# Kernel optimization log

Hardware: AMD Instinct MI355X
Metric: run time of the kernel (lower is better)

Reference implementation:

```python
import jax, jax.numpy as jnp
import numpy as np
import math

B, T, D, H = 4, 2048, 1024, 16
DH = D // H

def setup_inputs() -> dict:
    key = jax.random.key(0)
    ks = jax.random.split(key, 5)
    scale = 1.0 / math.sqrt(D)
    x = jax.random.normal(ks[0], (B, T, D), dtype=jnp.float32)
    Wq = jax.random.normal(ks[1], (D, D), dtype=jnp.float32) * scale
    Wk = jax.random.normal(ks[2], (D, D), dtype=jnp.float32) * scale
    Wv = jax.random.normal(ks[3], (D, D), dtype=jnp.float32) * scale
    Wo = jax.random.normal(ks[4], (D, D), dtype=jnp.float32) * scale
    mask = jnp.tril(jnp.ones((T, T), dtype=jnp.int32))  # causal, 1=keep
    return {"x": x, "mask": mask, "Wq": Wq, "Wk": Wk, "Wv": Wv, "Wo": Wo}

def reference(x, mask, Wq, Wk, Wv, Wo):
    Bx, Tx, Dx = x.shape
    # nn.Linear(bias=False): y = x @ W.T
    q = (x @ Wq.T).reshape(Bx, Tx, H, DH).transpose(0, 2, 1, 3)  # [B,H,T,dh]
    k = (x @ Wk.T).reshape(Bx, Tx, H, DH).transpose(0, 2, 1, 3)
    v = (x @ Wv.T).reshape(Bx, Tx, H, DH).transpose(0, 2, 1, 3)
    scores = jnp.einsum('bhqd,bhkd->bhqk', q, k) / math.sqrt(DH)
    m = mask[None, None, :, :]  # [1,1,T,T]
    scores = scores + (m == 0).astype(scores.dtype) * -1e9
    attn = jax.nn.softmax(scores, axis=-1)  # stable (max-subtract) like original
    out = jnp.einsum('bhqk,bhkd->bhqd', attn, v)
    out = out.transpose(0, 2, 1, 3).reshape(Bx, Tx, Dx)
    return out @ Wo.T
```

## Files before the change

### kernel.cpp

```cpp
#include <hip/hip_runtime.h>
#include <stdint.h>

#define B_  4
#define T_  2048
#define D_  1024
#define H_  16
#define DH_ 64

typedef unsigned short u16;
typedef __attribute__((ext_vector_type(8))) short bf16x8;
typedef __attribute__((ext_vector_type(8))) unsigned short u16x8;
typedef __attribute__((ext_vector_type(4))) unsigned short u16x4;
typedef __attribute__((ext_vector_type(4))) float f32x4;

#define NT_ ((size_t)B_ * T_ * D_)
#define QSCALE 0.18033688011112043f

__device__ __forceinline__ u16 f2bf(float f) {
    union { float f; uint32_t u; } v; v.f = f;
    uint32_t r = v.u + 0x7FFFu + ((v.u >> 16) & 1u);
    return (u16)(r >> 16);
}

__device__ __forceinline__ uint32_t pack2(float lo, float hi) {
    union { float f; uint32_t u; } a, b; a.f = lo; b.f = hi;
    return __builtin_amdgcn_perm(b.u, a.u, 0x07060302u);
}

__device__ __forceinline__ void gl2lds16(const u16* g, u16* l) {
    __builtin_amdgcn_global_load_lds(
        (const __attribute__((address_space(1))) unsigned int*)g,
        (__attribute__((address_space(3))) unsigned int*)l,
        16, 0, 0);
}

__global__ __launch_bounds__(256) void cvt_x_kernel(
    const float* __restrict__ src, u16* __restrict__ dst, int n8)
{
    int i = blockIdx.x * 256 + threadIdx.x;
    if (i >= n8) return;
    f32x4 a = ((const f32x4*)src)[2 * i];
    f32x4 b = ((const f32x4*)src)[2 * i + 1];
    u16x8 o;
    o[0]=f2bf(a[0]); o[1]=f2bf(a[1]); o[2]=f2bf(a[2]); o[3]=f2bf(a[3]);
    o[4]=f2bf(b[0]); o[5]=f2bf(b[1]); o[6]=f2bf(b[2]); o[7]=f2bf(b[3]);
    ((u16x8*)dst)[i] = o;
}

__global__ __launch_bounds__(256) void cvt_w_kernel(
    const float* __restrict__ w0, const float* __restrict__ w1,
    const float* __restrict__ w2, const float* __restrict__ w3,
    u16* __restrict__ dst)
{
    const float* src = (blockIdx.y == 0) ? w0 : (blockIdx.y == 1) ? w1
                     : (blockIdx.y == 2) ? w2 : w3;
    u16* d = dst + (size_t)blockIdx.y * (D_ * D_);
    int i = blockIdx.x * 256 + threadIdx.x;
    f32x4 a = ((const f32x4*)src)[2 * i];
    f32x4 b = ((const f32x4*)src)[2 * i + 1];
    u16x8 o;
    o[0]=f2bf(a[0]); o[1]=f2bf(a[1]); o[2]=f2bf(a[2]); o[3]=f2bf(a[3]);
    o[4]=f2bf(b[0]); o[5]=f2bf(b[1]); o[6]=f2bf(b[2]); o[7]=f2bf(b[3]);
    ((u16x8*)d)[i] = o;
}

template<int OUT_MODE>
__global__ __launch_bounds__(256) void gemm_bt_kernel(
    const u16* __restrict__ X, const u16* __restrict__ W,
    void* __restrict__ C, int M, int N, int K)
{
    __shared__ __align__(16) u16 As[128 * 64];
    __shared__ __align__(16) u16 Bs[128 * 64];

    const int tid  = threadIdx.x;
    const int wave = tid >> 6;
    const int lane = tid & 63;
    const int lq = lane >> 4;
    const int lm = lane & 15;
    const int m0 = blockIdx.x * 128;
    const int n0 = blockIdx.y * 128;
    const int wm = (wave & 1) * 64;
    const int wn = (wave >> 1) * 64;

    f32x4 acc[4][4] = {};

    const int r0 = wave * 32 + (lane >> 3);
    const int c0 = (lane & 7) * 8;
    const u16* gA = X + (size_t)(m0 + r0) * K + c0;
    const u16* gB = W + (size_t)(n0 + r0) * K + c0;
    u16* lA = As + wave * 32 * 64;
    u16* lB = Bs + wave * 32 * 64;

    for (int k0 = 0; k0 < K; k0 += 64) {
#pragma unroll
        for (int p = 0; p < 4; ++p) {
            gl2lds16(gA + (size_t)p * 8 * K + k0, lA + p * 8 * 64);
            gl2lds16(gB + (size_t)p * 8 * K + k0, lB + p * 8 * 64);
        }
        __syncthreads();
#pragma unroll
        for (int ks = 0; ks < 2; ++ks) {
            bf16x8 af[4], bfr[4];
#pragma unroll
            for (int t = 0; t < 4; ++t)
                af[t] = *(const bf16x8*)(As + (wm + t * 16 + lm) * 64 + ks * 32 + lq * 8);
#pragma unroll
            for (int t = 0; t < 4; ++t)
                bfr[t] = *(const bf16x8*)(Bs + (wn + t * 16 + lm) * 64 + ks * 32 + lq * 8);
#pragma unroll
            for (int i = 0; i < 4; ++i)
#pragma unroll
                for (int j = 0; j < 4; ++j)
                    acc[i][j] = __builtin_amdgcn_mfma_f32_16x16x32_bf16(
                        af[i], bfr[j], acc[i][j], 0, 0, 0);
        }
        __syncthreads();
    }

    const int region = n0 >> 10;
#pragma unroll
    for (int i = 0; i < 4; ++i)
#pragma unroll
        for (int j = 0; j < 4; ++j) {
            int rowb = m0 + wm + i * 16 + lq * 4;
            int col  = n0 + wn + j * 16 + lm;
            if (OUT_MODE == 2) {
#pragma unroll
                for (int r = 0; r < 4; ++r)
                    ((float*)C)[(size_t)(rowb + r) * N + col] = acc[i][j][r];
            } else {
                u16* Qp = (u16*)C;
                int colr = col & 1023;
                if (region == 0) {
#pragma unroll
                    for (int r = 0; r < 4; ++r)
                        Qp[(size_t)(rowb + r) * D_ + colr] = f2bf(acc[i][j][r] * QSCALE);
                } else if (region == 1) {
#pragma unroll
                    for (int r = 0; r < 4; ++r)
                        (Qp + NT_)[(size_t)(rowb + r) * D_ + colr] = f2bf(acc[i][j][r]);
                } else {
                    int b = rowb >> 11, t = rowb & (T_ - 1);
                    u16x4 pk;
#pragma unroll
                    for (int r = 0; r < 4; ++r) pk[r] = f2bf(acc[i][j][r]);
                    *(u16x4*)((Qp + 2 * NT_) + ((size_t)b * D_ + colr) * T_ + t) = pk;
                }
            }
        }
}

__global__ __launch_bounds__(128) void attn_kernel(
    const u16* __restrict__ Qg, const u16* __restrict__ Kg,
    const u16* __restrict__ Vtg, u16* __restrict__ Og)
{
    __shared__ __align__(16) u16 Pl[2 * 64 * 40];
    __shared__ __align__(16) float Oc[16 * 64 * 4];
    __shared__ __align__(16) float Lc[4 * 64];

    const int tid  = threadIdx.x;
    const int wave = tid >> 6;
    const int lane = tid & 63;
    const int lq = lane >> 4, lm = lane & 15;
    const int id = blockIdx.x;
    const int xs = id & 7;
    const int k8 = id >> 3;
    const int bh = xs + 8 * (k8 & 7);
    const int pi = k8 >> 3;
    const int b = bh >> 4, h = bh & 15;

    const size_t batchoff = (size_t)b * T_ * D_;
    const size_t headoff  = (size_t)h * DH_;
    const size_t vbase    = (size_t)bh * DH_ * T_;

    u16* pw = Pl + wave * 64 * 40;

#pragma unroll 1
    for (int ph = 0; ph < 2; ++ph) {
        const int qj  = ph ? (31 - pi) : pi;
        const int qw  = qj * 64;
        const int ktd = qj >> 1;
        const int odd = qj & 1;

        bf16x8 aq[4][2];
#pragma unroll
        for (int qf = 0; qf < 4; ++qf) {
            const u16* qrow = Qg + batchoff + (size_t)(qw + qf * 16 + lm) * D_ + headoff;
            aq[qf][0] = *(const bf16x8*)(qrow + lq * 8);
            aq[qf][1] = *(const bf16x8*)(qrow + 32 + lq * 8);
        }

        f32x4 oaccT[4][4] = {};
        float l_lane[4] = {0.f, 0.f, 0.f, 0.f};

#pragma unroll 1
        for (int kt = wave; kt <= ktd; kt += 2) {
            const bool diag = (kt == ktd);
            const int ksmax = diag ? (odd ? 3 : 1) : 3;

#pragma unroll
            for (int c = 0; c < 4; ++c) {
                if (c <= ksmax) {
#pragma unroll
                    for (int t = 0; t < 2; ++t) {
                        const int mt = 2 * c + t;
                        const u16* krow = Kg + batchoff
                            + (size_t)(kt * 128 + mt * 16 + lm) * D_ + headoff;
                        bf16x8 kf0 = *(const bf16x8*)(krow + lq * 8);
                        bf16x8 kf1 = *(const bf16x8*)(krow + 32 + lq * 8);
                        f32x4 s[4];
#pragma unroll
                        for (int qf = 0; qf < 4; ++qf) {
                            s[qf] = f32x4{0.f, 0.f, 0.f, 0.f};
                            s[qf] = __builtin_amdgcn_mfma_f32_16x16x32_bf16(
                                kf0, aq[qf][0], s[qf], 0, 0, 0);
                            s[qf] = __builtin_amdgcn_mfma_f32_16x16x32_bf16(
                                kf1, aq[qf][1], s[qf], 0, 0, 0);
                        }
                        if (diag) {
                            int keyb = kt * 128 + mt * 16 + lq * 4;
#pragma unroll
                            for (int qf = 0; qf < 4; ++qf) {
                                int query = qw + qf * 16 + lm;
#pragma unroll
                                for (int r = 0; r < 4; ++r)
                                    if (keyb + r > query) s[qf][r] = -1e9f;
                            }
                        }
#pragma unroll
                        for (int qf = 0; qf < 4; ++qf) {
                            float p0 = __builtin_amdgcn_exp2f(s[qf][0]);
                            float p1 = __builtin_amdgcn_exp2f(s[qf][1]);
                            float p2 = __builtin_amdgcn_exp2f(s[qf][2]);
                            float p3 = __builtin_amdgcn_exp2f(s[qf][3]);
                            l_lane[qf] += (p0 + p1) + (p2 + p3);
                            uint2 d; d.x = pack2(p0, p1); d.y = pack2(p2, p3);
                            *(uint2*)(pw + (qf * 16 + lm) * 40 + t * 16 + lq * 4) = d;
                        }
                    }

                    bf16x8 pf[4];
#pragma unroll
                    for (int qf = 0; qf < 4; ++qf)
                        pf[qf] = *(const bf16x8*)(pw + (qf * 16 + lm) * 40 + lq * 8);
#pragma unroll
                    for (int mo = 0; mo < 4; ++mo) {
                        const u16* vrow = Vtg + vbase
                            + (size_t)(mo * 16 + lm) * T_ + kt * 128 + c * 32;
                        bf16x8 vf = *(const bf16x8*)(vrow + lq * 8);
#pragma unroll
                        for (int qf = 0; qf < 4; ++qf)
                            oaccT[qf][mo] = __builtin_amdgcn_mfma_f32_16x16x32_bf16(
                                vf, pf[qf], oaccT[qf][mo], 0, 0, 0);
                    }
                }
            }
        }

        if (wave == 1) {
#pragma unroll
            for (int qf = 0; qf < 4; ++qf) {
#pragma unroll
                for (int mo = 0; mo < 4; ++mo)
                    *(f32x4*)&Oc[((qf * 4 + mo) * 64 + lane) * 4] = oaccT[qf][mo];
                Lc[qf * 64 + lane] = l_lane[qf];
            }
        }
        __syncthreads();
        if (wave == 0) {
#pragma unroll
            for (int qf = 0; qf < 4; ++qf) {
#pragma unroll
                for (int mo = 0; mo < 4; ++mo) {
                    f32x4 o = *(const f32x4*)&Oc[((qf * 4 + mo) * 64 + lane) * 4];
#pragma unroll
                    for (int r = 0; r < 4; ++r) oaccT[qf][mo][r] += o[r];
                }
                l_lane[qf] += Lc[qf * 64 + lane];
            }
#pragma unroll
            for (int qf = 0; qf < 4; ++qf) {
                float l = l_lane[qf];
                l += __shfl_xor(l, 16, 64);
                l += __shfl_xor(l, 32, 64);
                float inv = 1.0f / l;
                int row = qw + qf * 16 + lm;
                u16* obase = Og + batchoff + (size_t)row * D_ + headoff;
#pragma unroll
                for (int mo = 0; mo < 4; ++mo) {
                    uint2 d;
                    d.x = pack2(oaccT[qf][mo][0] * inv, oaccT[qf][mo][1] * inv);
                    d.y = pack2(oaccT[qf][mo][2] * inv, oaccT[qf][mo][3] * inv);
                    *(uint2*)(obase + mo * 16 + lq * 4) = d;
                }
            }
        }
        __syncthreads();
    }
}

extern "C" void kernel_launch(void* const* d_in, const int* in_sizes, int n_in,
                              void* d_out, int out_size, void* d_ws, size_t ws_size,
                              hipStream_t stream)
{
    const float* x  = (const float*)d_in[0];
    const float* Wq = (const float*)d_in[2];
    const float* Wk = (const float*)d_in[3];
    const float* Wv = (const float*)d_in[4];
    const float* Wo = (const float*)d_in[5];

    const size_t DD = (size_t)D_ * D_;
    u16* Qb  = (u16*)d_ws;
    u16* Kb  = Qb + NT_;
    u16* Vb  = Kb + NT_;
    u16* Ob  = Vb + NT_;
    u16* xb  = Ob + NT_;
    u16* wb  = xb + NT_;

    const int M = B_ * T_;

    cvt_x_kernel<<<dim3((int)(NT_ / 8 / 256)), 256, 0, stream>>>(x, xb, (int)(NT_ / 8));
    cvt_w_kernel<<<dim3((int)(DD / 8 / 256), 4), 256, 0, stream>>>(Wq, Wk, Wv, Wo, wb);

    gemm_bt_kernel<3><<<dim3(M / 128, 3 * D_ / 128), 256, 0, stream>>>(
        xb, wb, Qb, M, 3 * D_, D_);

    attn_kernel<<<dim3(1024), 128, 0, stream>>>(Qb, Kb, Vb, Ob);

    gemm_bt_kernel<2><<<dim3(M / 128, D_ / 128), 256, 0, stream>>>(
        Ob, wb + 3 * DD, d_out, M, D_, D_);
}
```

Measured before the change: 289.5 us.

## Rewrite projection GEMM as 256x256 8-wave double-buffered pipelined kernel

```diff
diff --git a/kernel.cpp b/kernel.cpp
--- a/kernel.cpp
+++ b/kernel.cpp
@@ -33,6 +33,8 @@
         (__attribute__((address_space(3))) unsigned int*)l,
         16, 0, 0);
 }
+
+#define VMCNT(n) asm volatile("s_waitcnt vmcnt(" #n ")" ::: "memory")
 
 __global__ __launch_bounds__(256) void cvt_x_kernel(
     const float* __restrict__ src, u16* __restrict__ dst, int n8)
@@ -65,65 +67,129 @@
 }
 
 template<int OUT_MODE>
-__global__ __launch_bounds__(256) void gemm_bt_kernel(
+__global__ __launch_bounds__(512) void gemm8_kernel(
     const u16* __restrict__ X, const u16* __restrict__ W,
     void* __restrict__ C, int M, int N, int K)
 {
-    __shared__ __align__(16) u16 As[128 * 64];
-    __shared__ __align__(16) u16 Bs[128 * 64];
+    __shared__ __align__(16) u16 Ab2[2][256 * 64];
+    __shared__ __align__(16) u16 Bb2[2][256 * 64];
 
     const int tid  = threadIdx.x;
     const int wave = tid >> 6;
     const int lane = tid & 63;
-    const int lq = lane >> 4;
-    const int lm = lane & 15;
-    const int m0 = blockIdx.x * 128;
-    const int n0 = blockIdx.y * 128;
-    const int wm = (wave & 1) * 64;
-    const int wn = (wave >> 1) * 64;
-
-    f32x4 acc[4][4] = {};
-
-    const int r0 = wave * 32 + (lane >> 3);
-    const int c0 = (lane & 7) * 8;
-    const u16* gA = X + (size_t)(m0 + r0) * K + c0;
-    const u16* gB = W + (size_t)(n0 + r0) * K + c0;
-    u16* lA = As + wave * 32 * 64;
-    u16* lB = Bs + wave * 32 * 64;
-
-    for (int k0 = 0; k0 < K; k0 += 64) {
-#pragma unroll
-        for (int p = 0; p < 4; ++p) {
-            gl2lds16(gA + (size_t)p * 8 * K + k0, lA + p * 8 * 64);
-            gl2lds16(gB + (size_t)p * 8 * K + k0, lB + p * 8 * 64);
-        }
-        __syncthreads();
-#pragma unroll
-        for (int ks = 0; ks < 2; ++ks) {
-            bf16x8 af[4], bfr[4];
-#pragma unroll
-            for (int t = 0; t < 4; ++t)
-                af[t] = *(const bf16x8*)(As + (wm + t * 16 + lm) * 64 + ks * 32 + lq * 8);
-#pragma unroll
-            for (int t = 0; t < 4; ++t)
-                bfr[t] = *(const bf16x8*)(Bs + (wn + t * 16 + lm) * 64 + ks * 32 + lq * 8);
-#pragma unroll
-            for (int i = 0; i < 4; ++i)
+    const int lq = lane >> 4, lm = lane & 15;
+    const int wm = wave >> 2;
+    const int wn = wave & 3;
+
+    const int GX  = M >> 8;
+    const int nwg = GX * (N >> 8);
+    const int cpx = nwg >> 3;
+    const int swz = ((int)blockIdx.x & 7) * cpx + ((int)blockIdx.x >> 3);
+    const int m0 = (swz % GX) << 8;
+    const int n0 = (swz / GX) << 8;
+
+    const int srow = wave * 8 + (lane >> 3);
+    const int scol = ((lane & 7) ^ (lane >> 3)) << 3;
+    const u16* gA = X + (size_t)(m0 + srow) * K + scol;
+    const u16* gB = W + (size_t)(n0 + srow) * K + scol;
+    const size_t rK64 = (size_t)64 * K;
+
+    const int swzr = (lm & 7) << 4;
+
+    f32x4 acc[8][4] = {};
+    const int NT = K >> 6;
+
+    gl2lds16(gA,            Ab2[0] + wave * 512);
+    gl2lds16(gA + rK64,     Ab2[0] + 4096  + wave * 512);
+    gl2lds16(gA + 2 * rK64, Ab2[0] + 8192  + wave * 512);
+    gl2lds16(gA + 3 * rK64, Ab2[0] + 12288 + wave * 512);
+    gl2lds16(gB,            Bb2[0] + wave * 512);
+    gl2lds16(gB + rK64,     Bb2[0] + 4096  + wave * 512);
+    gl2lds16(gB + 2 * rK64, Bb2[0] + 8192  + wave * 512);
+    gl2lds16(gB + 3 * rK64, Bb2[0] + 12288 + wave * 512);
+    gl2lds16(gB + 64,            Bb2[1] + wave * 512);
+    gl2lds16(gB + 64 + rK64,     Bb2[1] + 4096  + wave * 512);
+    gl2lds16(gB + 64 + 2 * rK64, Bb2[1] + 8192  + wave * 512);
+    gl2lds16(gB + 64 + 3 * rK64, Bb2[1] + 12288 + wave * 512);
+    VMCNT(4);
+    __builtin_amdgcn_s_barrier();
+
+#pragma unroll 1
+    for (int t = 0; t < NT; ++t) {
+        const u16* Ablds = Ab2[t & 1];
+        const u16* Bblds = Bb2[t & 1];
+        u16* Abn = Ab2[(t & 1) ^ 1];
+        u16* Bbc = Bb2[t & 1];
+        const bool stA = (t + 1 < NT);
+        const bool stB = (t + 2 < NT);
+        const u16* gAs = gA + (size_t)(t + 1) * 64;
+        const u16* gBs = gB + (size_t)(t + 2) * 64;
+        bf16x8 bq[4][2];
+#pragma unroll
+        for (int q = 0; q < 4; ++q) {
+            bf16x8 af[2][2];
+#pragma unroll
+            for (int i2 = 0; i2 < 2; ++i2)
+#pragma unroll
+                for (int ks = 0; ks < 2; ++ks) {
+                    int off = (wm * 128 + (2 * q + i2) * 16 + lm) * 128
+                            + ks * 64 + lq * 16;
+                    af[i2][ks] = *(const bf16x8*)((const char*)Ablds + (off ^ swzr));
+                }
+            if (q == 0) {
 #pragma unroll
                 for (int j = 0; j < 4; ++j)
-                    acc[i][j] = __builtin_amdgcn_mfma_f32_16x16x32_bf16(
-                        af[i], bfr[j], acc[i][j], 0, 0, 0);
-        }
-        __syncthreads();
+#pragma unroll
+                    for (int ks = 0; ks < 2; ++ks) {
+                        int off = (wn * 64 + j * 16 + lm) * 128
+                                + ks * 64 + lq * 16;
+                        bq[j][ks] = *(const bf16x8*)((const char*)Bblds + (off ^ swzr));
+                    }
+                if (stA) {
+                    gl2lds16(gAs,        Abn + wave * 512);
+                    gl2lds16(gAs + rK64, Abn + 4096 + wave * 512);
+                }
+            }
+            if (q == 1 && stA) {
+                gl2lds16(gAs + 2 * rK64, Abn + 8192  + wave * 512);
+                gl2lds16(gAs + 3 * rK64, Abn + 12288 + wave * 512);
+            }
+            if (q == 2 && stB) {
+                gl2lds16(gBs,        Bbc + wave * 512);
+                gl2lds16(gBs + rK64, Bbc + 4096 + wave * 512);
+            }
+            if (q == 3 && stB) {
+                gl2lds16(gBs + 2 * rK64, Bbc + 8192  + wave * 512);
+                gl2lds16(gBs + 3 * rK64, Bbc + 12288 + wave * 512);
+            }
+            __builtin_amdgcn_s_barrier();
+            asm volatile("s_waitcnt lgkmcnt(0)" ::: "memory");
+            __builtin_amdgcn_sched_barrier(0);
+            __builtin_amdgcn_s_setprio(1);
+#pragma unroll
+            for (int ks = 0; ks < 2; ++ks)
+#pragma unroll
+                for (int i2 = 0; i2 < 2; ++i2)
+#pragma unroll
+                    for (int j = 0; j < 4; ++j)
+                        acc[2 * q + i2][j] = __builtin_amdgcn_mfma_f32_16x16x32_bf16(
+                            af[i2][ks], bq[j][ks], acc[2 * q + i2][j], 0, 0, 0);
+            __builtin_amdgcn_s_setprio(0);
+            if (q == 3) {
+                if (stB)      { VMCNT(4); }
+                else if (stA) { VMCNT(0); }
+            }
+            __builtin_amdgcn_s_barrier();
+        }
     }
 
     const int region = n0 >> 10;
 #pragma unroll
-    for (int i = 0; i < 4; ++i)
+    for (int i = 0; i < 8; ++i)
 #pragma unroll
         for (int j = 0; j < 4; ++j) {
-            int rowb = m0 + wm + i * 16 + lq * 4;
-            int col  = n0 + wn + j * 16 + lm;
+            int rowb = m0 + wm * 128 + i * 16 + lq * 4;
+            int col  = n0 + wn * 64 + j * 16 + lm;
             if (OUT_MODE == 2) {
 #pragma unroll
                 for (int r = 0; r < 4; ++r)
@@ -140,11 +206,11 @@
                     for (int r = 0; r < 4; ++r)
                         (Qp + NT_)[(size_t)(rowb + r) * D_ + colr] = f2bf(acc[i][j][r]);
                 } else {
-                    int b = rowb >> 11, t = rowb & (T_ - 1);
+                    int b = rowb >> 11, tt = rowb & (T_ - 1);
                     u16x4 pk;
 #pragma unroll
                     for (int r = 0; r < 4; ++r) pk[r] = f2bf(acc[i][j][r]);
-                    *(u16x4*)((Qp + 2 * NT_) + ((size_t)b * D_ + colr) * T_ + t) = pk;
+                    *(u16x4*)((Qp + 2 * NT_) + ((size_t)b * D_ + colr) * T_ + tt) = pk;
                 }
             }
         }
@@ -322,11 +388,11 @@
     cvt_x_kernel<<<dim3((int)(NT_ / 8 / 256)), 256, 0, stream>>>(x, xb, (int)(NT_ / 8));
     cvt_w_kernel<<<dim3((int)(DD / 8 / 256), 4), 256, 0, stream>>>(Wq, Wk, Wv, Wo, wb);
 
-    gemm_bt_kernel<3><<<dim3(M / 128, 3 * D_ / 128), 256, 0, stream>>>(
+    gemm8_kernel<3><<<dim3((M / 256) * (3 * D_ / 256)), 512, 0, stream>>>(
         xb, wb, Qb, M, 3 * D_, D_);
 
     attn_kernel<<<dim3(1024), 128, 0, stream>>>(Qb, Kb, Vb, Ob);
 
-    gemm_bt_kernel<2><<<dim3(M / 128, D_ / 128), 256, 0, stream>>>(
+    gemm8_kernel<2><<<dim3((M / 256) * (D_ / 256)), 512, 0, stream>>>(
         Ob, wb + 3 * DD, d_out, M, D_, D_);
 }
```

New measurement: 287.9 us. About the same (-0.5%).

## Add 8-wave 256x192 pipelined GEMM for fused QKV projection

Applied to the files above, without the earlier changes.

```diff
diff --git a/kernel.cpp b/kernel.cpp
--- a/kernel.cpp
+++ b/kernel.cpp
@@ -32,6 +32,15 @@
         (const __attribute__((address_space(1))) unsigned int*)g,
         (__attribute__((address_space(3))) unsigned int*)l,
         16, 0, 0);
+}
+
+#define VMCNT(n) asm volatile("s_waitcnt vmcnt(" #n ")" ::: "memory")
+#define SB0()    __builtin_amdgcn_sched_barrier(0)
+
+__device__ __forceinline__ bf16x8 ldsrd(const u16* base, int row, int ks,
+                                        int lq, int swzr) {
+    int off = row * 128 + ks * 64 + lq * 16;
+    return *(const bf16x8*)((const char*)base + (off ^ swzr));
 }
 
 __global__ __launch_bounds__(256) void cvt_x_kernel(
@@ -65,9 +74,183 @@
 }
 
 template<int OUT_MODE>
+__global__ __launch_bounds__(512) void gemm8_kernel(
+    const u16* __restrict__ X, const u16* __restrict__ W,
+    void* __restrict__ C, int M, int N, int K)
+{
+    __shared__ __align__(16) u16 Ab2[2][256 * 64];
+    __shared__ __align__(16) u16 Bb2[2][192 * 64];
+
+    const int tid  = threadIdx.x;
+    const int wave = tid >> 6;
+    const int lane = tid & 63;
+    const int lq = lane >> 4, lm = lane & 15;
+    const int wm = wave >> 2;
+    const int wn = wave & 3;
+
+    const int xcd = (int)blockIdx.x & 7;
+    const int idx = (int)blockIdx.x >> 3;
+    const int m0 = (((xcd & 3) << 3) + (idx & 7)) << 8;
+    const int n0 = (((xcd >> 2) << 3) + (idx >> 3)) * 192;
+
+    const int srow = wave * 8 + (lane >> 3);
+    const int scol = ((lane & 7) ^ (lane >> 3)) << 3;
+    const u16* gA = X + (size_t)(m0 + srow) * K + scol;
+    const u16* gB = W + (size_t)(n0 + srow) * K + scol;
+    const size_t rK64 = (size_t)64 * K;
+
+    const int swzr = (lm & 7) << 4;
+
+    f32x4 acc[8][3] = {};
+    bf16x8 afA[2][2], afB[2][2];
+    bf16x8 bqA[3][2], bqB[3][2];
+    const int NT = K >> 6;
+
+    gl2lds16(gA,            (u16*)Ab2[0] + wave * 512);
+    gl2lds16(gA + rK64,     (u16*)Ab2[0] + 4096  + wave * 512);
+    gl2lds16(gA + 2 * rK64, (u16*)Ab2[0] + 8192  + wave * 512);
+    gl2lds16(gA + 3 * rK64, (u16*)Ab2[0] + 12288 + wave * 512);
+    gl2lds16(gB,            (u16*)Bb2[0] + wave * 512);
+    gl2lds16(gB + rK64,     (u16*)Bb2[0] + 4096  + wave * 512);
+    gl2lds16(gB + 2 * rK64, (u16*)Bb2[0] + 8192  + wave * 512);
+    gl2lds16(gB + 64,            (u16*)Bb2[1] + wave * 512);
+    gl2lds16(gB + 64 + rK64,     (u16*)Bb2[1] + 4096  + wave * 512);
+    gl2lds16(gB + 64 + 2 * rK64, (u16*)Bb2[1] + 8192  + wave * 512);
+    VMCNT(3);
+    __builtin_amdgcn_s_barrier();
+#pragma unroll
+    for (int i2 = 0; i2 < 2; ++i2)
+#pragma unroll
+        for (int ks = 0; ks < 2; ++ks)
+            afA[i2][ks] = ldsrd(Ab2[0], wm * 128 + i2 * 16 + lm, ks, lq, swzr);
+#pragma unroll
+    for (int j = 0; j < 3; ++j)
+#pragma unroll
+        for (int ks = 0; ks < 2; ++ks)
+            bqA[j][ks] = ldsrd(Bb2[0], wn * 48 + j * 16 + lm, ks, lq, swzr);
+
+    auto tile_body = [&](int t, bf16x8 (&bqU)[3][2], bf16x8 (&bqF)[3][2])
+        __attribute__((always_inline)) -> void {
+        const u16* Ac = Ab2[t & 1];
+        const u16* An = Ab2[(t + 1) & 1];
+        const u16* Bn = Bb2[(t + 1) & 1];
+        u16* Abn = (u16*)Ab2[(t + 1) & 1];
+        u16* Bbc = (u16*)Bb2[t & 1];
+        const bool stA = (t + 1 < NT);
+        const bool stB = (t + 2 < NT);
+        const u16* gAs = gA + (size_t)(t + 1) * 64;
+        const u16* gBs = gB + (size_t)(t + 2) * 64;
+
+#define MFMA_PH(Q, AF, BQ)                                                  \
+        __builtin_amdgcn_s_setprio(1);                                      \
+        _Pragma("unroll")                                                   \
+        for (int ks = 0; ks < 2; ++ks)                                      \
+            _Pragma("unroll")                                               \
+            for (int i2 = 0; i2 < 2; ++i2)                                  \
+                _Pragma("unroll")                                           \
+                for (int j = 0; j < 3; ++j)                                 \
+                    acc[2 * (Q) + i2][j] =                                  \
+                        __builtin_amdgcn_mfma_f32_16x16x32_bf16(            \
+                            AF[i2][ks], BQ[j][ks], acc[2 * (Q) + i2][j],    \
+                            0, 0, 0);                                       \
+        __builtin_amdgcn_s_setprio(0);
+
+#define RD_AF(SET, P, BASE)                                                 \
+        _Pragma("unroll")                                                   \
+        for (int i2 = 0; i2 < 2; ++i2)                                      \
+            _Pragma("unroll")                                               \
+            for (int ks = 0; ks < 2; ++ks)                                  \
+                SET[i2][ks] = ldsrd(BASE,                                   \
+                    wm * 128 + (2 * (P) + i2) * 16 + lm, ks, lq, swzr);
+
+        RD_AF(afB, 1, Ac);
+        if (stA) {
+            gl2lds16(gAs,        Abn + wave * 512);
+            gl2lds16(gAs + rK64, Abn + 4096 + wave * 512);
+        }
+        SB0(); __builtin_amdgcn_s_barrier(); SB0();
+        MFMA_PH(0, afA, bqU); SB0();
+        __builtin_amdgcn_s_barrier();
+
+        RD_AF(afA, 2, Ac);
+        if (stA) {
+            gl2lds16(gAs + 2 * rK64, Abn + 8192  + wave * 512);
+            gl2lds16(gAs + 3 * rK64, Abn + 12288 + wave * 512);
+        }
+        SB0(); __builtin_amdgcn_s_barrier(); SB0();
+        MFMA_PH(1, afB, bqU); SB0();
+        __builtin_amdgcn_s_barrier();
+
+        RD_AF(afB, 3, Ac);
+        if (stB) {
+            gl2lds16(gBs,        Bbc + wave * 512);
+            gl2lds16(gBs + rK64, Bbc + 4096 + wave * 512);
+        }
+        SB0(); __builtin_amdgcn_s_barrier(); SB0();
+        MFMA_PH(2, afA, bqU); SB0();
+        if (stB)      { VMCNT(2); }
+        else if (stA) { VMCNT(0); }
+        __builtin_amdgcn_s_barrier();
+
+        if (stA) {
+            RD_AF(afA, 0, An);
+#pragma unroll
+            for (int j = 0; j < 3; ++j)
+#pragma unroll
+                for (int ks = 0; ks < 2; ++ks)
+                    bqF[j][ks] = ldsrd(Bn, wn * 48 + j * 16 + lm, ks, lq, swzr);
+        }
+        if (stB)
+            gl2lds16(gBs + 2 * rK64, Bbc + 8192 + wave * 512);
+        SB0(); __builtin_amdgcn_s_barrier(); SB0();
+        MFMA_PH(3, afB, bqU); SB0();
+        __builtin_amdgcn_s_barrier();
+#undef RD_AF
+#undef MFMA_PH
+    };
+
+#pragma unroll 1
+    for (int tt = 0; tt < NT; tt += 2) {
+        tile_body(tt,     bqA, bqB);
+        tile_body(tt + 1, bqB, bqA);
+    }
+
+#pragma unroll
+    for (int i = 0; i < 8; ++i)
+#pragma unroll
+        for (int j = 0; j < 3; ++j) {
+            int rowb = m0 + wm * 128 + i * 16 + lq * 4;
+            int col  = n0 + wn * 48 + j * 16 + lm;
+            if (OUT_MODE == 2) {
+#pragma unroll
+                for (int r = 0; r < 4; ++r)
+                    ((float*)C)[(size_t)(rowb + r) * N + col] = acc[i][j][r];
+            } else {
+                u16* Qp = (u16*)C;
+                int region = col >> 10;
+                int colr = col & 1023;
+                if (region == 0) {
+#pragma unroll
+                    for (int r = 0; r < 4; ++r)
+                        Qp[(size_t)(rowb + r) * D_ + colr] = f2bf(acc[i][j][r] * QSCALE);
+                } else if (region == 1) {
+#pragma unroll
+                    for (int r = 0; r < 4; ++r)
+                        (Qp + NT_)[(size_t)(rowb + r) * D_ + colr] = f2bf(acc[i][j][r]);
+                } else {
+                    int b = rowb >> 11, tt2 = rowb & (T_ - 1);
+                    u16x4 pk;
+#pragma unroll
+                    for (int r = 0; r < 4; ++r) pk[r] = f2bf(acc[i][j][r]);
+                    *(u16x4*)((Qp + 2 * NT_) + ((size_t)b * D_ + colr) * T_ + tt2) = pk;
+                }
+            }
+        }
+}
+
 __global__ __launch_bounds__(256) void gemm_bt_kernel(
     const u16* __restrict__ X, const u16* __restrict__ W,
-    void* __restrict__ C, int M, int N, int K)
+    float* __restrict__ C, int M, int N, int K)
 {
     __shared__ __align__(16) u16 As[128 * 64];
     __shared__ __align__(16) u16 Bs[128 * 64];
@@ -117,36 +300,15 @@
         __syncthreads();
     }
 
-    const int region = n0 >> 10;
 #pragma unroll
     for (int i = 0; i < 4; ++i)
 #pragma unroll
         for (int j = 0; j < 4; ++j) {
             int rowb = m0 + wm + i * 16 + lq * 4;
             int col  = n0 + wn + j * 16 + lm;
-            if (OUT_MODE == 2) {
-#pragma unroll
-                for (int r = 0; r < 4; ++r)
-                    ((float*)C)[(size_t)(rowb + r) * N + col] = acc[i][j][r];
-            } else {
-                u16* Qp = (u16*)C;
-                int colr = col & 1023;
-                if (region == 0) {
-#pragma unroll
-                    for (int r = 0; r < 4; ++r)
-                        Qp[(size_t)(rowb + r) * D_ + colr] = f2bf(acc[i][j][r] * QSCALE);
-                } else if (region == 1) {
-#pragma unroll
-                    for (int r = 0; r < 4; ++r)
-                        (Qp + NT_)[(size_t)(rowb + r) * D_ + colr] = f2bf(acc[i][j][r]);
-                } else {
-                    int b = rowb >> 11, t = rowb & (T_ - 1);
-                    u16x4 pk;
-#pragma unroll
-                    for (int r = 0; r < 4; ++r) pk[r] = f2bf(acc[i][j][r]);
-                    *(u16x4*)((Qp + 2 * NT_) + ((size_t)b * D_ + colr) * T_ + t) = pk;
-                }
-            }
+#pragma unroll
+            for (int r = 0; r < 4; ++r)
+                C[(size_t)(rowb + r) * N + col] = acc[i][j][r];
         }
 }
 
@@ -322,11 +484,11 @@
     cvt_x_kernel<<<dim3((int)(NT_ / 8 / 256)), 256, 0, stream>>>(x, xb, (int)(NT_ / 8));
     cvt_w_kernel<<<dim3((int)(DD / 8 / 256), 4), 256, 0, stream>>>(Wq, Wk, Wv, Wo, wb);
 
-    gemm_bt_kernel<3><<<dim3(M / 128, 3 * D_ / 128), 256, 0, stream>>>(
+    gemm8_kernel<3><<<dim3((M / 256) * (3 * D_ / 192)), 512, 0, stream>>>(
         xb, wb, Qb, M, 3 * D_, D_);
 
     attn_kernel<<<dim3(1024), 128, 0, stream>>>(Qb, Kb, Vb, Ob);
 
-    gemm_bt_kernel<2><<<dim3(M / 128, D_ / 128), 256, 0, stream>>>(
-        Ob, wb + 3 * DD, d_out, M, D_, D_);
-}
+    gemm_bt_kernel<<<dim3(M / 128, D_ / 128), 256, 0, stream>>>(
+        Ob, wb + 3 * DD, (float*)d_out, M, D_, D_);
+}
```

After: 271.3 us. -6.3%, faster.
